# Optimization experiments

Measured on AMD Instinct MI355X. Metric: run time of the kernel, lower is better.

## Reference

```python
import jax, jax.numpy as jnp
import numpy as np


def setup_inputs() -> dict:
    key = jax.random.key(0)
    k1, k2 = jax.random.split(key)
    D = 512
    B, N = 32, 512
    panel_embeddings = jax.random.normal(k1, (B, N, D), dtype=jnp.float32)
    # nn.Bilinear(D, D, 1) weight: (1, D, D) -> squeeze to (D, D); bias: scalar
    bound = 1.0 / np.sqrt(D)
    W = jax.random.uniform(k2, (D, D), dtype=jnp.float32, minval=-bound, maxval=bound)
    b = jnp.float32(0.0)
    return {"panel_embeddings": panel_embeddings, "W": W, "b": b}


def reference(panel_embeddings, W, b):
    # score[b,i,j] = x_i^T W x_j + b, with diagonal forced to 0 (loop skips i==j)
    xw = jnp.einsum('bid,de->bie', panel_embeddings, W)          # (B, N, D)
    scores = jnp.einsum('bie,bje->bij', xw, panel_embeddings) + b  # (B, N, N)
    N = panel_embeddings.shape[1]
    mask = ~jnp.eye(N, dtype=bool)
    return jnp.where(mask, scores, jnp.zeros_like(scores))
```

## Files before the change

kernel.cpp:

```cpp
#include <hip/hip_runtime.h>
#include <stdint.h>

#define BATCH 32
#define NDIM 512
#define DDIM 512
#define XELEMS (BATCH * NDIM * DDIM)
#define WELEMS (DDIM * DDIM)

typedef _Float16 f16x8 __attribute__((ext_vector_type(8)));
typedef _Float16 f16x4v __attribute__((ext_vector_type(4)));
typedef float f32x4 __attribute__((ext_vector_type(4)));

__device__ __forceinline__ void gl_lds16(const _Float16* g, _Float16* l) {
    __builtin_amdgcn_global_load_lds(
        (const __attribute__((address_space(1))) unsigned int*)(g),
        (__attribute__((address_space(3))) unsigned int*)(l),
        16, 0, 0);
}

#define WAITVM(N) do { asm volatile("s_waitcnt vmcnt(" #N ")" ::: "memory"); \
                       __builtin_amdgcn_sched_barrier(0); } while (0)

__global__ __launch_bounds__(256) void prep(const float4* __restrict__ X4,
                                            f16x4v* __restrict__ Xh4,
                                            const float* __restrict__ W,
                                            _Float16* __restrict__ Wt) {
    __shared__ float tile[32][33];
    int bid = blockIdx.x;
    if (bid < XELEMS / 4 / 256) {
        int i = bid * 256 + threadIdx.x;
        float4 v = X4[i];
        f16x4v o;
        o.x = (_Float16)v.x;
        o.y = (_Float16)v.y;
        o.z = (_Float16)v.z;
        o.w = (_Float16)v.w;
        Xh4[i] = o;
    } else {
        int t = bid - XELEMS / 4 / 256;
        int bx = t & 15;
        int by = t >> 4;
        int tx = threadIdx.x & 31;
        int ty = threadIdx.x >> 5;
        for (int r = ty; r < 32; r += 8)
            tile[r][tx] = W[(by * 32 + r) * DDIM + bx * 32 + tx];
        __syncthreads();
        for (int r = ty; r < 32; r += 8)
            Wt[(size_t)(bx * 32 + r) * DDIM + by * 32 + tx] = (_Float16)tile[tx][r];
    }
}

__global__ __launch_bounds__(512) void fused(const _Float16* __restrict__ Xh,
                                             const _Float16* __restrict__ Wt,
                                             float* __restrict__ Sout,
                                             const float* __restrict__ bias_ptr) {
    __shared__ __align__(16) _Float16 AY[64 * 512];
    __shared__ __align__(16) _Float16 Bs[2][8 * 2048];

    const int tid  = threadIdx.x;
    const int lane = tid & 63;
    const int wv   = tid >> 6;
    const int quad = lane >> 4;
    const int l16  = lane & 15;

    const int lr2 = lane >> 2;
    const int lc2 = lane & 3;
    const int lk2 = (lc2 ^ ((lr2 >> 1) & 3)) * 8;

    const int paK = (quad ^ ((l16 >> 1) & 3)) * 8;

    const int blk   = blockIdx.x;
    const int batch = blk & 31;
    const int r0    = (blk >> 5) * 64;

    const _Float16* Xb = Xh + (size_t)batch * (NDIM * DDIM);

    f32x4 acc[4][4];
#pragma unroll
    for (int i = 0; i < 4; ++i)
#pragma unroll
        for (int j = 0; j < 4; ++j)
            acc[i][j] = (f32x4){0.f, 0.f, 0.f, 0.f};

#pragma unroll
    for (int c = 0; c < 8; ++c) {
        const int kt = wv * 2 + (c >> 2);
        const int rc = c & 3;
        gl_lds16(Xb + (size_t)(r0 + rc * 16 + lr2) * DDIM + kt * 32 + lk2,
                 &AY[(kt * 4 + rc) * 512]);
    }
#pragma unroll
    for (int t = 0; t < 4; ++t)
        gl_lds16(Wt + (size_t)(wv * 64 + t * 16 + lr2) * DDIM + lk2,
                 &Bs[0][wv * 2048 + t * 512]);
    WAITVM(4);
    __builtin_amdgcn_s_barrier();

#pragma unroll
    for (int it = 0; it < 15; ++it) {
        const int buf = it & 1;
        const int k0 = (it + 1) * 32;
#pragma unroll
        for (int t = 0; t < 4; ++t)
            gl_lds16(Wt + (size_t)(wv * 64 + t * 16 + lr2) * DDIM + k0 + lk2,
                     &Bs[buf ^ 1][wv * 2048 + t * 512]);
        WAITVM(4);
        f16x8 a[4], b[4];
#pragma unroll
        for (int mt = 0; mt < 4; ++mt)
            a[mt] = *(const f16x8*)&AY[(it * 4 + mt) * 512 + l16 * 32 + paK];
#pragma unroll
        for (int nt = 0; nt < 4; ++nt)
            b[nt] = *(const f16x8*)&Bs[buf][wv * 2048 + nt * 512 + l16 * 32 + paK];
#pragma unroll
        for (int mt = 0; mt < 4; ++mt)
#pragma unroll
            for (int nt = 0; nt < 4; ++nt)
                acc[mt][nt] = __builtin_amdgcn_mfma_f32_16x16x32_f16(
                    a[mt], b[nt], acc[mt][nt], 0, 0, 0);
    }
    {
        const int buf = 15 & 1;
#pragma unroll
        for (int t = 0; t < 4; ++t)
            gl_lds16(Xb + (size_t)(wv * 64 + t * 16 + lr2) * DDIM + lk2,
                     &Bs[buf ^ 1][wv * 2048 + t * 512]);
        WAITVM(4);
        f16x8 a[4], b[4];
#pragma unroll
        for (int mt = 0; mt < 4; ++mt)
            a[mt] = *(const f16x8*)&AY[(15 * 4 + mt) * 512 + l16 * 32 + paK];
#pragma unroll
        for (int nt = 0; nt < 4; ++nt)
            b[nt] = *(const f16x8*)&Bs[buf][wv * 2048 + nt * 512 + l16 * 32 + paK];
#pragma unroll
        for (int mt = 0; mt < 4; ++mt)
#pragma unroll
            for (int nt = 0; nt < 4; ++nt)
                acc[mt][nt] = __builtin_amdgcn_mfma_f32_16x16x32_f16(
                    a[mt], b[nt], acc[mt][nt], 0, 0, 0);
    }

    __builtin_amdgcn_s_barrier();
#pragma unroll
    for (int mt = 0; mt < 4; ++mt)
#pragma unroll
        for (int nt = 0; nt < 4; ++nt)
#pragma unroll
            for (int r = 0; r < 4; ++r) {
                int i = mt * 16 + quad * 4 + r;
                int e = wv * 64 + nt * 16 + l16;
                int c = e >> 3, j = e & 7;
                AY[i * 512 + (((c ^ (i & 7)) << 3) | j)] = (_Float16)acc[mt][nt][r];
            }
    asm volatile("s_waitcnt lgkmcnt(0)" ::: "memory");
    __builtin_amdgcn_s_barrier();

#pragma unroll
    for (int i = 0; i < 4; ++i)
#pragma unroll
        for (int j = 0; j < 4; ++j)
            acc[i][j] = (f32x4){0.f, 0.f, 0.f, 0.f};

#pragma unroll
    for (int it = 0; it < 15; ++it) {
        const int buf = it & 1;
        const int e0 = (it + 1) * 32;
#pragma unroll
        for (int t = 0; t < 4; ++t)
            gl_lds16(Xb + (size_t)(wv * 64 + t * 16 + lr2) * DDIM + e0 + lk2,
                     &Bs[buf ^ 1][wv * 2048 + t * 512]);
        WAITVM(4);
        const int pay = (((it * 4 + quad) ^ (l16 & 7)) * 8);
        f16x8 a[4], b[4];
#pragma unroll
        for (int mt = 0; mt < 4; ++mt)
            a[mt] = *(const f16x8*)&AY[(mt * 16 + l16) * 512 + pay];
#pragma unroll
        for (int nt = 0; nt < 4; ++nt)
            b[nt] = *(const f16x8*)&Bs[buf][wv * 2048 + nt * 512 + l16 * 32 + paK];
#pragma unroll
        for (int mt = 0; mt < 4; ++mt)
#pragma unroll
            for (int nt = 0; nt < 4; ++nt)
                acc[mt][nt] = __builtin_amdgcn_mfma_f32_16x16x32_f16(
                    a[mt], b[nt], acc[mt][nt], 0, 0, 0);
    }
    {
        const int buf = 15 & 1;
        WAITVM(0);
        const int pay = (((15 * 4 + quad) ^ (l16 & 7)) * 8);
        f16x8 a[4], b[4];
#pragma unroll
        for (int mt = 0; mt < 4; ++mt)
            a[mt] = *(const f16x8*)&AY[(mt * 16 + l16) * 512 + pay];
#pragma unroll
        for (int nt = 0; nt < 4; ++nt)
            b[nt] = *(const f16x8*)&Bs[buf][wv * 2048 + nt * 512 + l16 * 32 + paK];
#pragma unroll
        for (int mt = 0; mt < 4; ++mt)
#pragma unroll
            for (int nt = 0; nt < 4; ++nt)
                acc[mt][nt] = __builtin_amdgcn_mfma_f32_16x16x32_f16(
                    a[mt], b[nt], acc[mt][nt], 0, 0, 0);
    }

    const float bias = bias_ptr[0];
#pragma unroll
    for (int mt = 0; mt < 4; ++mt)
#pragma unroll
        for (int nt = 0; nt < 4; ++nt)
#pragma unroll
            for (int r = 0; r < 4; ++r) {
                int gi = r0 + mt * 16 + quad * 4 + r;
                int gj = wv * 64 + nt * 16 + l16;
                float v = acc[mt][nt][r] + bias;
                if (gi == gj) v = 0.f;
                Sout[((size_t)batch * NDIM + gi) * NDIM + gj] = v;
            }
}

extern "C" void kernel_launch(void* const* d_in, const int* in_sizes, int n_in,
                              void* d_out, int out_size, void* d_ws, size_t ws_size,
                              hipStream_t stream) {
    const float* X  = (const float*)d_in[0];
    const float* W  = (const float*)d_in[1];
    const float* bp = (const float*)d_in[2];
    float* out = (float*)d_out;

    _Float16* Xh = (_Float16*)d_ws;
    _Float16* Wt = Xh + XELEMS;

    prep<<<XELEMS / 4 / 256 + 256, 256, 0, stream>>>((const float4*)X, (f16x4v*)Xh, W, Wt);

    fused<<<256, 512, 0, stream>>>(Xh, Wt, out, bp);

    (void)in_sizes; (void)n_in; (void)out_size; (void)ws_size;
}
```

Measured before the change: 110.0 us.

## Pre-tile and pre-swizzle fp16 X and W into contiguous 1KB chunks in prep

The prep kernel now writes X and transposed W in a tiled layout: each 16-row by 32-k tile is stored as a contiguous 1KB chunk with the LDS XOR swizzle already applied. The fused kernel's global-to-LDS loads then read fully contiguous 1KB per wave instead of 16 strided row segments. This is meant to improve global load coalescing and cut address arithmetic. In exchange, prep does strided 32-byte reads per lane, and only half of its W-transpose threads do the writes.

```diff
diff --git a/kernel.cpp b/kernel.cpp
--- a/kernel.cpp
+++ b/kernel.cpp
@@ -5,11 +5,18 @@
 #define NDIM 512
 #define DDIM 512
 #define XELEMS (BATCH * NDIM * DDIM)
-#define WELEMS (DDIM * DDIM)
 
 typedef _Float16 f16x8 __attribute__((ext_vector_type(8)));
-typedef _Float16 f16x4v __attribute__((ext_vector_type(4)));
 typedef float f32x4 __attribute__((ext_vector_type(4)));
+
+__device__ __forceinline__ f16x8 cvt8(float4 u0, float4 u1) {
+    f16x8 r;
+    r[0] = (_Float16)u0.x; r[1] = (_Float16)u0.y;
+    r[2] = (_Float16)u0.z; r[3] = (_Float16)u0.w;
+    r[4] = (_Float16)u1.x; r[5] = (_Float16)u1.y;
+    r[6] = (_Float16)u1.z; r[7] = (_Float16)u1.w;
+    return r;
+}
 
 __device__ __forceinline__ void gl_lds16(const _Float16* g, _Float16* l) {
     __builtin_amdgcn_global_load_lds(
@@ -21,37 +28,52 @@
 #define WAITVM(N) do { asm volatile("s_waitcnt vmcnt(" #N ")" ::: "memory"); \
                        __builtin_amdgcn_sched_barrier(0); } while (0)
 
-__global__ __launch_bounds__(256) void prep(const float4* __restrict__ X4,
-                                            f16x4v* __restrict__ Xh4,
+
+__global__ __launch_bounds__(256) void prep(const float* __restrict__ X,
+                                            _Float16* __restrict__ XhT,
                                             const float* __restrict__ W,
-                                            _Float16* __restrict__ Wt) {
-    __shared__ float tile[32][33];
+                                            _Float16* __restrict__ WtT) {
     int bid = blockIdx.x;
-    if (bid < XELEMS / 4 / 256) {
-        int i = bid * 256 + threadIdx.x;
-        float4 v = X4[i];
-        f16x4v o;
-        o.x = (_Float16)v.x;
-        o.y = (_Float16)v.y;
-        o.z = (_Float16)v.z;
-        o.w = (_Float16)v.w;
-        Xh4[i] = o;
+    if (bid < 4096) {
+        int g    = bid * 4 + (threadIdx.x >> 6);
+        int lane = threadIdx.x & 63;
+        int b  = g >> 9;
+        int kt = (g >> 5) & 15;
+        int ch = g & 31;
+        int r = lane >> 2, s = lane & 3;
+        int col = kt * 32 + ((s ^ ((r >> 1) & 3)) << 3);
+        const float* src = X + ((size_t)(b * 512 + ch * 16 + r)) * DDIM + col;
+        float4 u0 = *(const float4*)src;
+        float4 u1 = *(const float4*)(src + 4);
+        *(f16x8*)&XhT[(size_t)g * 512 + lane * 8] = cvt8(u0, u1);
     } else {
-        int t = bid - XELEMS / 4 / 256;
+        __shared__ float tile[32][33];
+        int t  = bid - 4096;
         int bx = t & 15;
         int by = t >> 4;
         int tx = threadIdx.x & 31;
         int ty = threadIdx.x >> 5;
-        for (int r = ty; r < 32; r += 8)
-            tile[r][tx] = W[(by * 32 + r) * DDIM + bx * 32 + tx];
+        for (int rr = ty; rr < 32; rr += 8)
+            tile[rr][tx] = W[(by * 32 + rr) * DDIM + bx * 32 + tx];
         __syncthreads();
-        for (int r = ty; r < 32; r += 8)
-            Wt[(size_t)(bx * 32 + r) * DDIM + by * 32 + tx] = (_Float16)tile[tx][r];
-    }
-}
-
-__global__ __launch_bounds__(512) void fused(const _Float16* __restrict__ Xh,
-                                             const _Float16* __restrict__ Wt,
+        int idx = threadIdx.x;
+        if (idx < 128) {
+            int er = idx >> 2;
+            int sp = idx & 3;
+            int rr = er & 15;
+            int sl = sp ^ ((rr >> 1) & 3);
+            f16x8 v;
+#pragma unroll
+            for (int j = 0; j < 8; ++j)
+                v[j] = (_Float16)tile[sl * 8 + j][er];
+            int ch = bx * 2 + (er >> 4);
+            *(f16x8*)&WtT[((size_t)(by * 32 + ch)) * 512 + rr * 32 + sp * 8] = v;
+        }
+    }
+}
+
+__global__ __launch_bounds__(512) void fused(const _Float16* __restrict__ XhT,
+                                             const _Float16* __restrict__ WtT,
                                              float* __restrict__ Sout,
                                              const float* __restrict__ bias_ptr) {
     __shared__ __align__(16) _Float16 AY[64 * 512];
@@ -62,18 +84,16 @@
     const int wv   = tid >> 6;
     const int quad = lane >> 4;
     const int l16  = lane & 15;
-
-    const int lr2 = lane >> 2;
-    const int lc2 = lane & 3;
-    const int lk2 = (lc2 ^ ((lr2 >> 1) & 3)) * 8;
+    const int l8   = lane * 8;
 
     const int paK = (quad ^ ((l16 >> 1) & 3)) * 8;
 
     const int blk   = blockIdx.x;
     const int batch = blk & 31;
     const int r0    = (blk >> 5) * 64;
-
-    const _Float16* Xb = Xh + (size_t)batch * (NDIM * DDIM);
+    const int ch0   = r0 >> 4;
+
+    const _Float16* Xt = XhT + (size_t)(batch * 16) * 32 * 512;
 
     f32x4 acc[4][4];
 #pragma unroll
@@ -86,12 +106,12 @@
     for (int c = 0; c < 8; ++c) {
         const int kt = wv * 2 + (c >> 2);
         const int rc = c & 3;
-        gl_lds16(Xb + (size_t)(r0 + rc * 16 + lr2) * DDIM + kt * 32 + lk2,
+        gl_lds16(Xt + ((size_t)(kt * 32 + ch0 + rc)) * 512 + l8,
                  &AY[(kt * 4 + rc) * 512]);
     }
 #pragma unroll
     for (int t = 0; t < 4; ++t)
-        gl_lds16(Wt + (size_t)(wv * 64 + t * 16 + lr2) * DDIM + lk2,
+        gl_lds16(WtT + ((size_t)(0 * 32 + wv * 4 + t)) * 512 + l8,
                  &Bs[0][wv * 2048 + t * 512]);
     WAITVM(4);
     __builtin_amdgcn_s_barrier();
@@ -99,10 +119,10 @@
 #pragma unroll
     for (int it = 0; it < 15; ++it) {
         const int buf = it & 1;
-        const int k0 = (it + 1) * 32;
+        const int ktn = it + 1;
 #pragma unroll
         for (int t = 0; t < 4; ++t)
-            gl_lds16(Wt + (size_t)(wv * 64 + t * 16 + lr2) * DDIM + k0 + lk2,
+            gl_lds16(WtT + ((size_t)(ktn * 32 + wv * 4 + t)) * 512 + l8,
                      &Bs[buf ^ 1][wv * 2048 + t * 512]);
         WAITVM(4);
         f16x8 a[4], b[4];
@@ -123,7 +143,7 @@
         const int buf = 15 & 1;
 #pragma unroll
         for (int t = 0; t < 4; ++t)
-            gl_lds16(Xb + (size_t)(wv * 64 + t * 16 + lr2) * DDIM + lk2,
+            gl_lds16(Xt + ((size_t)(0 * 32 + wv * 4 + t)) * 512 + l8,
                      &Bs[buf ^ 1][wv * 2048 + t * 512]);
         WAITVM(4);
         f16x8 a[4], b[4];
@@ -165,10 +185,10 @@
 #pragma unroll
     for (int it = 0; it < 15; ++it) {
         const int buf = it & 1;
-        const int e0 = (it + 1) * 32;
+        const int etn = it + 1;
 #pragma unroll
         for (int t = 0; t < 4; ++t)
-            gl_lds16(Xb + (size_t)(wv * 64 + t * 16 + lr2) * DDIM + e0 + lk2,
+            gl_lds16(Xt + ((size_t)(etn * 32 + wv * 4 + t)) * 512 + l8,
                      &Bs[buf ^ 1][wv * 2048 + t * 512]);
         WAITVM(4);
         const int pay = (((it * 4 + quad) ^ (l16 & 7)) * 8);
@@ -228,12 +248,12 @@
     const float* bp = (const float*)d_in[2];
     float* out = (float*)d_out;
 
-    _Float16* Xh = (_Float16*)d_ws;
-    _Float16* Wt = Xh + XELEMS;
-
-    prep<<<XELEMS / 4 / 256 + 256, 256, 0, stream>>>((const float4*)X, (f16x4v*)Xh, W, Wt);
-
-    fused<<<256, 512, 0, stream>>>(Xh, Wt, out, bp);
+    _Float16* XhT = (_Float16*)d_ws;
+    _Float16* WtT = XhT + XELEMS;
+
+    prep<<<4096 + 256, 256, 0, stream>>>(X, XhT, W, WtT);
+
+    fused<<<256, 512, 0, stream>>>(XhT, WtT, out, bp);
 
     (void)in_sizes; (void)n_in; (void)out_size; (void)ws_size;
 }
```

Result: faster. 107.0 us, median of 3 (-2.8%).
